# Kernel optimization log

Measured on AMD Instinct MI355X. Metric: run time of the kernel, lower is better.

The kernel has to match this reference:

```python
import jax, jax.numpy as jnp
import numpy as np


def setup_inputs() -> dict:
    key = jax.random.key(0)
    k1, k2 = jax.random.split(key)
    N = 2_000_000
    rotation = jax.random.normal(k1, (N, 3, 3), dtype=jnp.float32)
    # learned parameter: eye(3) + 0.001 * randn(3,3)
    mat = jnp.eye(3, dtype=jnp.float32) + 0.001 * jax.random.normal(k2, (3, 3), dtype=jnp.float32)
    return {"rotation": rotation, "mat": mat}


def reference(rotation, mat):
    # new_mat[n] = rotation[n] @ mat   (mat broadcast over the batch)
    new_mat = jnp.einsum('nab,bc->nac', rotation, mat)
    # batched 3x3 SVD; polar orthogonal factor U @ V^T
    U, S, Vh = jnp.linalg.svd(new_mat, full_matrices=False)
    out = jnp.einsum('nab,nbc->nac', U, Vh)  # Vh is already V^T
    logdet = jnp.zeros((rotation.shape[0],), dtype=rotation.dtype)
    return out, logdet
```

## Files before the change

### kernel.cpp

```cpp
#include <hip/hip_runtime.h>
#include <math.h>

constexpr int BLOCK = 256;

__global__ __launch_bounds__(BLOCK) void polar3x3_kernel(
    const float* __restrict__ rot,
    const float* __restrict__ mat,
    float* __restrict__ outq,
    float* __restrict__ logdet,
    int N)
{
    __shared__ float lds[BLOCK * 9];
    const int tid = threadIdx.x;
    const long long base = (long long)blockIdx.x * BLOCK;
    int rem = N - (int)base;
    const int nmat = rem < BLOCK ? rem : BLOCK;
    const int nflt = nmat * 9;
    const int nv4 = nflt >> 2;

    const float* gsrc = rot + base * 9;
    {
        const float4* g4 = (const float4*)gsrc;
        float4* l4 = (float4*)lds;
        for (int i = tid; i < nv4; i += BLOCK) l4[i] = g4[i];
        for (int i = (nv4 << 2) + tid; i < nflt; i += BLOCK) lds[i] = gsrc[i];
    }
    __syncthreads();

    const double m0 = (double)mat[0], m1 = (double)mat[1], m2 = (double)mat[2];
    const double m3 = (double)mat[3], m4 = (double)mat[4], m5 = (double)mat[5];
    const double m6 = (double)mat[6], m7 = (double)mat[7], m8 = (double)mat[8];

    const bool active = tid < nmat;
    float x0=1.f,x1=0.f,x2=0.f,x3=0.f,x4=1.f,x5=0.f,x6=0.f,x7=0.f,x8=1.f;

    if (active) {
        const float* r = &lds[tid * 9];
        const double r0=r[0], r1=r[1], r2=r[2], r3=r[3], r4=r[4],
                     r5=r[5], r6=r[6], r7=r[7], r8=r[8];
        const double a0 = r0*m0 + r1*m3 + r2*m6;
        const double a1 = r0*m1 + r1*m4 + r2*m7;
        const double a2 = r0*m2 + r1*m5 + r2*m8;
        const double a3 = r3*m0 + r4*m3 + r5*m6;
        const double a4 = r3*m1 + r4*m4 + r5*m7;
        const double a5 = r3*m2 + r4*m5 + r5*m8;
        const double a6 = r6*m0 + r7*m3 + r8*m6;
        const double a7 = r6*m1 + r7*m4 + r8*m7;
        const double a8 = r6*m2 + r7*m5 + r8*m8;

        const double c0 = a4*a8 - a5*a7;
        const double c1 = a5*a6 - a3*a8;
        const double c2 = a3*a7 - a4*a6;
        const double c3 = a2*a7 - a1*a8;
        const double c4 = a0*a8 - a2*a6;
        const double c5 = a1*a6 - a0*a7;
        const double c6 = a1*a5 - a2*a4;
        const double c7 = a2*a3 - a0*a5;
        const double c8 = a0*a4 - a1*a3;
        double det = a0*c0 + a1*c1 + a2*c2;
        double adet = fabs(det);
        adet = fmax(adet, 1e-300);
        det = copysign(adet, det);
        const double nX = sqrt(a0*a0+a1*a1+a2*a2+a3*a3+a4*a4+a5*a5+a6*a6+a7*a7+a8*a8);
        const double nC = sqrt(c0*c0+c1*c1+c2*c2+c3*c3+c4*c4+c5*c5+c6*c6+c7*c7+c8*c8);
        const double g = sqrt(nC / (adet * nX));
        const double s = 0.5 * g;
        const double t = 0.5 / (g * det);
        const double y0 = s*a0 + t*c0, y1 = s*a1 + t*c1, y2 = s*a2 + t*c2;
        const double y3 = s*a3 + t*c3, y4 = s*a4 + t*c4, y5 = s*a5 + t*c5;
        const double y6 = s*a6 + t*c6, y7 = s*a7 + t*c7, y8 = s*a8 + t*c8;
        const double inv = 1.0 / sqrt(y0*y0+y1*y1+y2*y2+y3*y3+y4*y4+y5*y5+y6*y6+y7*y7+y8*y8);
        x0 = (float)(y0*inv); x1 = (float)(y1*inv); x2 = (float)(y2*inv);
        x3 = (float)(y3*inv); x4 = (float)(y4*inv); x5 = (float)(y5*inv);
        x6 = (float)(y6*inv); x7 = (float)(y7*inv); x8 = (float)(y8*inv);
    }
    __syncthreads();

    #pragma unroll
    for (int it = 0; it < 6; ++it) {
        const float c0 = x4*x8 - x5*x7;
        const float c1 = x5*x6 - x3*x8;
        const float c2 = x3*x7 - x4*x6;
        const float c3 = x2*x7 - x1*x8;
        const float c4 = x0*x8 - x2*x6;
        const float c5 = x1*x6 - x0*x7;
        const float c6 = x1*x5 - x2*x4;
        const float c7 = x2*x3 - x0*x5;
        const float c8 = x0*x4 - x1*x3;
        float det = x0*c0 + x1*c1 + x2*c2;
        float adet = fmaxf(fabsf(det), 1e-30f);
        det = copysignf(adet, det);
        const float nX = sqrtf(x0*x0+x1*x1+x2*x2+x3*x3+x4*x4+x5*x5+x6*x6+x7*x7+x8*x8);
        const float nC = sqrtf(c0*c0+c1*c1+c2*c2+c3*c3+c4*c4+c5*c5+c6*c6+c7*c7+c8*c8);
        const float g = sqrtf(nC / (adet * nX));
        const float s = 0.5f * g;
        const float t = 0.5f / (g * det);
        x0 = s*x0 + t*c0; x1 = s*x1 + t*c1; x2 = s*x2 + t*c2;
        x3 = s*x3 + t*c3; x4 = s*x4 + t*c4; x5 = s*x5 + t*c5;
        x6 = s*x6 + t*c6; x7 = s*x7 + t*c7; x8 = s*x8 + t*c8;
    }

    if (active) {
        float* w = &lds[tid * 9];
        w[0]=x0; w[1]=x1; w[2]=x2; w[3]=x3; w[4]=x4;
        w[5]=x5; w[6]=x6; w[7]=x7; w[8]=x8;
    }
    __syncthreads();

    float* gdst = outq + base * 9;
    {
        float4* g4 = (float4*)gdst;
        const float4* l4 = (const float4*)lds;
        for (int i = tid; i < nv4; i += BLOCK) g4[i] = l4[i];
        for (int i = (nv4 << 2) + tid; i < nflt; i += BLOCK) gdst[i] = lds[i];
    }

    if (base + tid < N) logdet[base + tid] = 0.0f;
}

extern "C" void kernel_launch(void* const* d_in, const int* in_sizes, int n_in,
                              void* d_out, int out_size, void* d_ws, size_t ws_size,
                              hipStream_t stream) {
    const float* rot = (const float*)d_in[0];
    const float* mat = (const float*)d_in[1];
    float* out = (float*)d_out;
    const int N = in_sizes[0] / 9;
    float* logdet = out + (long long)N * 9;
    const int nblocks = (N + BLOCK - 1) / BLOCK;
    polar3x3_kernel<<<nblocks, BLOCK, 0, stream>>>(rot, mat, out, logdet, N);
}
```

Before: 163.4 us.

## Drop LDS staging and fp64 first iteration; use fast fp32 intrinsics

Each thread now loads its 3x3 rotation directly from global memory instead of staging it through LDS, which removes the block-wide syncs. The fp64 first Newton polar step is replaced by an fp32 one seeded with a determinant computed in double as det(R)*det(M). The iteration is rewritten with fma and hardware rcp/sqrt/rsq intrinsics in place of IEEE divides and sqrts. The risks are stride-9 uncoalesced global accesses and lower accuracy for ill-conditioned matrices, since the fp64 pre-step is gone and the same 6 iterations remain.

```diff
diff --git a/kernel.cpp b/kernel.cpp
--- a/kernel.cpp
+++ b/kernel.cpp
@@ -10,112 +10,74 @@
     float* __restrict__ logdet,
     int N)
 {
-    __shared__ float lds[BLOCK * 9];
-    const int tid = threadIdx.x;
-    const long long base = (long long)blockIdx.x * BLOCK;
-    int rem = N - (int)base;
-    const int nmat = rem < BLOCK ? rem : BLOCK;
-    const int nflt = nmat * 9;
-    const int nv4 = nflt >> 2;
+    const long long idx = (long long)blockIdx.x * BLOCK + threadIdx.x;
+    if (idx >= N) return;
 
-    const float* gsrc = rot + base * 9;
-    {
-        const float4* g4 = (const float4*)gsrc;
-        float4* l4 = (float4*)lds;
-        for (int i = tid; i < nv4; i += BLOCK) l4[i] = g4[i];
-        for (int i = (nv4 << 2) + tid; i < nflt; i += BLOCK) lds[i] = gsrc[i];
-    }
-    __syncthreads();
+    const float* rp = rot + idx * 9;
+    const float r0=rp[0], r1=rp[1], r2=rp[2], r3=rp[3], r4=rp[4],
+                r5=rp[5], r6=rp[6], r7=rp[7], r8=rp[8];
 
-    const double m0 = (double)mat[0], m1 = (double)mat[1], m2 = (double)mat[2];
-    const double m3 = (double)mat[3], m4 = (double)mat[4], m5 = (double)mat[5];
-    const double m6 = (double)mat[6], m7 = (double)mat[7], m8 = (double)mat[8];
+    const float m0=mat[0], m1=mat[1], m2=mat[2], m3=mat[3], m4=mat[4],
+                m5=mat[5], m6=mat[6], m7=mat[7], m8=mat[8];
 
-    const bool active = tid < nmat;
-    float x0=1.f,x1=0.f,x2=0.f,x3=0.f,x4=1.f,x5=0.f,x6=0.f,x7=0.f,x8=1.f;
+    float x0 = fmaf(r0,m0, fmaf(r1,m3, r2*m6));
+    float x1 = fmaf(r0,m1, fmaf(r1,m4, r2*m7));
+    float x2 = fmaf(r0,m2, fmaf(r1,m5, r2*m8));
+    float x3 = fmaf(r3,m0, fmaf(r4,m3, r5*m6));
+    float x4 = fmaf(r3,m1, fmaf(r4,m4, r5*m7));
+    float x5 = fmaf(r3,m2, fmaf(r4,m5, r5*m8));
+    float x6 = fmaf(r6,m0, fmaf(r7,m3, r8*m6));
+    float x7 = fmaf(r6,m1, fmaf(r7,m4, r8*m7));
+    float x8 = fmaf(r6,m2, fmaf(r7,m5, r8*m8));
 
-    if (active) {
-        const float* r = &lds[tid * 9];
-        const double r0=r[0], r1=r[1], r2=r[2], r3=r[3], r4=r[4],
-                     r5=r[5], r6=r[6], r7=r[7], r8=r[8];
-        const double a0 = r0*m0 + r1*m3 + r2*m6;
-        const double a1 = r0*m1 + r1*m4 + r2*m7;
-        const double a2 = r0*m2 + r1*m5 + r2*m8;
-        const double a3 = r3*m0 + r4*m3 + r5*m6;
-        const double a4 = r3*m1 + r4*m4 + r5*m7;
-        const double a5 = r3*m2 + r4*m5 + r5*m8;
-        const double a6 = r6*m0 + r7*m3 + r8*m6;
-        const double a7 = r6*m1 + r7*m4 + r8*m7;
-        const double a8 = r6*m2 + r7*m5 + r8*m8;
-
-        const double c0 = a4*a8 - a5*a7;
-        const double c1 = a5*a6 - a3*a8;
-        const double c2 = a3*a7 - a4*a6;
-        const double c3 = a2*a7 - a1*a8;
-        const double c4 = a0*a8 - a2*a6;
-        const double c5 = a1*a6 - a0*a7;
-        const double c6 = a1*a5 - a2*a4;
-        const double c7 = a2*a3 - a0*a5;
-        const double c8 = a0*a4 - a1*a3;
-        double det = a0*c0 + a1*c1 + a2*c2;
-        double adet = fabs(det);
-        adet = fmax(adet, 1e-300);
-        det = copysign(adet, det);
-        const double nX = sqrt(a0*a0+a1*a1+a2*a2+a3*a3+a4*a4+a5*a5+a6*a6+a7*a7+a8*a8);
-        const double nC = sqrt(c0*c0+c1*c1+c2*c2+c3*c3+c4*c4+c5*c5+c6*c6+c7*c7+c8*c8);
-        const double g = sqrt(nC / (adet * nX));
-        const double s = 0.5 * g;
-        const double t = 0.5 / (g * det);
-        const double y0 = s*a0 + t*c0, y1 = s*a1 + t*c1, y2 = s*a2 + t*c2;
-        const double y3 = s*a3 + t*c3, y4 = s*a4 + t*c4, y5 = s*a5 + t*c5;
-        const double y6 = s*a6 + t*c6, y7 = s*a7 + t*c7, y8 = s*a8 + t*c8;
-        const double inv = 1.0 / sqrt(y0*y0+y1*y1+y2*y2+y3*y3+y4*y4+y5*y5+y6*y6+y7*y7+y8*y8);
-        x0 = (float)(y0*inv); x1 = (float)(y1*inv); x2 = (float)(y2*inv);
-        x3 = (float)(y3*inv); x4 = (float)(y4*inv); x5 = (float)(y5*inv);
-        x6 = (float)(y6*inv); x7 = (float)(y7*inv); x8 = (float)(y8*inv);
-    }
-    __syncthreads();
+    const double dR = (double)r0*((double)r4*r8 - (double)r5*r7)
+                    - (double)r1*((double)r3*r8 - (double)r5*r6)
+                    + (double)r2*((double)r3*r7 - (double)r4*r6);
+    const double dM = (double)m0*((double)m4*m8 - (double)m5*m7)
+                    - (double)m1*((double)m3*m8 - (double)m5*m6)
+                    + (double)m2*((double)m3*m7 - (double)m4*m6);
+    const float detA = (float)(dR * dM);
 
     #pragma unroll
     for (int it = 0; it < 6; ++it) {
-        const float c0 = x4*x8 - x5*x7;
-        const float c1 = x5*x6 - x3*x8;
-        const float c2 = x3*x7 - x4*x6;
-        const float c3 = x2*x7 - x1*x8;
-        const float c4 = x0*x8 - x2*x6;
-        const float c5 = x1*x6 - x0*x7;
-        const float c6 = x1*x5 - x2*x4;
-        const float c7 = x2*x3 - x0*x5;
-        const float c8 = x0*x4 - x1*x3;
-        float det = x0*c0 + x1*c1 + x2*c2;
-        float adet = fmaxf(fabsf(det), 1e-30f);
-        det = copysignf(adet, det);
-        const float nX = sqrtf(x0*x0+x1*x1+x2*x2+x3*x3+x4*x4+x5*x5+x6*x6+x7*x7+x8*x8);
-        const float nC = sqrtf(c0*c0+c1*c1+c2*c2+c3*c3+c4*c4+c5*c5+c6*c6+c7*c7+c8*c8);
-        const float g = sqrtf(nC / (adet * nX));
+        const float c0 = fmaf(x4,x8, -x5*x7);
+        const float c1 = fmaf(x5,x6, -x3*x8);
+        const float c2 = fmaf(x3,x7, -x4*x6);
+        const float c3 = fmaf(x2,x7, -x1*x8);
+        const float c4 = fmaf(x0,x8, -x2*x6);
+        const float c5 = fmaf(x1,x6, -x0*x7);
+        const float c6 = fmaf(x1,x5, -x2*x4);
+        const float c7 = fmaf(x2,x3, -x0*x5);
+        const float c8 = fmaf(x0,x4, -x1*x3);
+        const float det = (it == 0) ? detA
+                        : fmaf(x0,c0, fmaf(x1,c1, x2*c2));
+        const float adet = fmaxf(fabsf(det), 1e-30f);
+        const float sdet = copysignf(adet, det);
+        float nX2 = x0*x0;
+        nX2 = fmaf(x1,x1, nX2); nX2 = fmaf(x2,x2, nX2);
+        nX2 = fmaf(x3,x3, nX2); nX2 = fmaf(x4,x4, nX2);
+        nX2 = fmaf(x5,x5, nX2); nX2 = fmaf(x6,x6, nX2);
+        nX2 = fmaf(x7,x7, nX2); nX2 = fmaf(x8,x8, nX2);
+        float nC2 = c0*c0;
+        nC2 = fmaf(c1,c1, nC2); nC2 = fmaf(c2,c2, nC2);
+        nC2 = fmaf(c3,c3, nC2); nC2 = fmaf(c4,c4, nC2);
+        nC2 = fmaf(c5,c5, nC2); nC2 = fmaf(c6,c6, nC2);
+        nC2 = fmaf(c7,c7, nC2); nC2 = fmaf(c8,c8, nC2);
+        const float rr = nC2 * __builtin_amdgcn_rcpf(nX2);
+        const float g  = __builtin_amdgcn_sqrtf(__builtin_amdgcn_sqrtf(rr))
+                       * __builtin_amdgcn_rsqf(adet);
         const float s = 0.5f * g;
-        const float t = 0.5f / (g * det);
-        x0 = s*x0 + t*c0; x1 = s*x1 + t*c1; x2 = s*x2 + t*c2;
-        x3 = s*x3 + t*c3; x4 = s*x4 + t*c4; x5 = s*x5 + t*c5;
-        x6 = s*x6 + t*c6; x7 = s*x7 + t*c7; x8 = s*x8 + t*c8;
+        const float t = 0.5f * __builtin_amdgcn_rcpf(g * sdet);
+        x0 = fmaf(s,x0, t*c0); x1 = fmaf(s,x1, t*c1); x2 = fmaf(s,x2, t*c2);
+        x3 = fmaf(s,x3, t*c3); x4 = fmaf(s,x4, t*c4); x5 = fmaf(s,x5, t*c5);
+        x6 = fmaf(s,x6, t*c6); x7 = fmaf(s,x7, t*c7); x8 = fmaf(s,x8, t*c8);
     }
 
-    if (active) {
-        float* w = &lds[tid * 9];
-        w[0]=x0; w[1]=x1; w[2]=x2; w[3]=x3; w[4]=x4;
-        w[5]=x5; w[6]=x6; w[7]=x7; w[8]=x8;
-    }
-    __syncthreads();
+    float* op = outq + idx * 9;
+    op[0]=x0; op[1]=x1; op[2]=x2; op[3]=x3; op[4]=x4;
+    op[5]=x5; op[6]=x6; op[7]=x7; op[8]=x8;
 
-    float* gdst = outq + base * 9;
-    {
-        float4* g4 = (float4*)gdst;
-        const float4* l4 = (const float4*)lds;
-        for (int i = tid; i < nv4; i += BLOCK) g4[i] = l4[i];
-        for (int i = (nv4 << 2) + tid; i < nflt; i += BLOCK) gdst[i] = lds[i];
-    }
-
-    if (base + tid < N) logdet[base + tid] = 0.0f;
+    logdet[idx] = 0.0f;
 }
 
 extern "C" void kernel_launch(void* const* d_in, const int* in_sizes, int n_in,
```

Result: faster. 139.3 us (-14.7%).
